# Kernel optimization log

Measured on AMD Instinct MI355X. Metric: run time of the kernel, lower is better.

Reference implementation:

```python
import math
import jax, jax.numpy as jnp
import numpy as np

E = 1024          # emb_size
H = 16            # num_heads
D = E // H        # head_dim
B, S = 4, 2048
DI = 64           # intent dim
K = 32            # num intent clusters
ASSIGN_W = 0.5
MU_W = 0.5
UNC_W = 0.5
EXPLORE_SCALE = 0.5
EXPLOIT_SCALE = 0.5
TEMP_MIN = 0.5
TEMP_MAX = 2.0


def setup_inputs() -> dict:
    key = jax.random.key(0)
    ks = jax.random.split(key, 16)
    inp = {
        "his_emb": jax.random.normal(ks[0], (B, S, E), dtype=jnp.float32),
        "src_key_padding_mask": jax.random.randint(ks[1], (B, S), 0, 2).astype(bool),
        "intent_mu": jax.random.normal(ks[2], (B, S, DI), dtype=jnp.float32),
        "intent_sigma": jax.random.uniform(ks[3], (B, S, DI), dtype=jnp.float32),
        "intent_assign": jax.random.uniform(ks[4], (B, S, K), dtype=jnp.float32),
        "explore": jax.random.uniform(ks[5], (B, S), dtype=jnp.float32),
        "exploit": jax.random.uniform(ks[6], (B, S), dtype=jnp.float32),
    }
    std = 0.02
    inp["Wq"] = jax.random.normal(ks[7], (E, E), dtype=jnp.float32) * std
    inp["bq"] = jnp.zeros((E,), dtype=jnp.float32)
    inp["Wk"] = jax.random.normal(ks[8], (E, E), dtype=jnp.float32) * std
    inp["bk"] = jnp.zeros((E,), dtype=jnp.float32)
    inp["Wv"] = jax.random.normal(ks[9], (E, E), dtype=jnp.float32) * std
    inp["bv"] = jnp.zeros((E,), dtype=jnp.float32)
    inp["Wo"] = jax.random.normal(ks[10], (E, E), dtype=jnp.float32) * std
    inp["bo"] = jnp.zeros((E,), dtype=jnp.float32)
    return inp


def _forward(his_emb, src_key_padding_mask, intent_mu, intent_sigma, intent_assign,
             explore, exploit, Wq, bq, Wk, bk, Wv, bv, Wo, bo):
    b, s, _ = his_emb.shape
    # projections -> [b, h, s, d]
    def proj(W, bias):
        return (his_emb @ W.T + bias).reshape(b, s, H, D).transpose(0, 2, 1, 3)
    q, k, v = proj(Wq, bq), proj(Wk, bk), proj(Wv, bv)

    logits = jnp.einsum("bhqd,bhkd->bhqk", q, k) / math.sqrt(D)  # [b,h,s,s]

    # intent bias [b, s, s]
    assign_sim = jnp.einsum("bqc,bkc->bqk", intent_assign, intent_assign)
    bias = ASSIGN_W * assign_sim
    # mean squared distance via expansion (avoids [b,s,s,DI] intermediate)
    sq = jnp.sum(intent_mu * intent_mu, axis=-1)  # [b,s]
    dot = jnp.einsum("bqd,bkd->bqk", intent_mu, intent_mu)
    mu_dist = (sq[:, :, None] + sq[:, None, :] - 2.0 * dot) / DI
    bias = bias - MU_W * mu_dist
    uncertainty = jnp.mean(intent_sigma, axis=-1)[:, None, :]  # [b,1,s] over keys
    bias = bias - UNC_W * uncertainty

    logits = logits + bias[:, None, :, :]

    attn_mask = src_key_padding_mask[:, None, None, :]  # [b,1,1,s]
    logits = jnp.where(attn_mask, -1e16, logits)

    # per-query temperature scaling
    temperature = 1.0 + EXPLORE_SCALE * explore - EXPLOIT_SCALE * exploit
    temperature = jnp.clip(temperature, TEMP_MIN, TEMP_MAX)
    temperature = jnp.where(src_key_padding_mask, 1.0, temperature)  # [b,s]
    logits = logits / temperature[:, None, :, None]

    probs = jax.nn.softmax(logits, axis=-1)
    probs = jnp.where(attn_mask, 0.0, probs)
    probs = probs / jnp.maximum(jnp.sum(probs, axis=-1, keepdims=True), 1e-8)

    out = jnp.einsum("bhqk,bhkd->bhqd", probs, v)
    out = out.transpose(0, 2, 1, 3).reshape(b, s, E)
    out = out @ Wo.T + bo
    return jnp.where(src_key_padding_mask[:, :, None], 0.0, out)


def reference(his_emb, src_key_padding_mask, intent_mu, intent_sigma, intent_assign,
              explore, exploit, Wq, bq, Wk, bk, Wv, bv, Wo, bo):
    return _forward(his_emb, src_key_padding_mask, intent_mu, intent_sigma,
                    intent_assign, explore, exploit, Wq, bq, Wk, bk, Wv, bv, Wo, bo)
```

## Files before the change

### kernel.cpp

```cpp
#include <hip/hip_runtime.h>
#include <hip/hip_bf16.h>
#include <stdint.h>
#include <stddef.h>

#define Bn 4
#define Sn 2048
#define En 1024
#define Hn 16
#define DIn 64
#define BSn (Bn*Sn)
#define L2E 1.44269504089f
#define SH8L 11.5415603271f

typedef __attribute__((ext_vector_type(8))) short short8;
typedef __attribute__((ext_vector_type(4))) short short4v;
typedef __attribute__((ext_vector_type(4))) float fx4;
typedef __attribute__((ext_vector_type(16))) float fx16;
typedef __attribute__((ext_vector_type(8))) _Float16 half8;
typedef __attribute__((ext_vector_type(2))) __fp16 fp16x2;
typedef __attribute__((ext_vector_type(4))) int ix4;

__device__ __forceinline__ short f2bf(float f){
  union U { __hip_bfloat16 h; short s; } u; u.h = __float2bfloat16(f); return u.s;
}
__device__ __forceinline__ short f2h(float f){
  _Float16 h = (_Float16)f; return __builtin_bit_cast(short, h);
}

__device__ __forceinline__ void async16(const void* g, void* l){
  __builtin_amdgcn_global_load_lds((const __attribute__((address_space(1))) unsigned int*)g,
                                   (__attribute__((address_space(3))) unsigned int*)l, 16, 0, 0);
}

__device__ __forceinline__ fx4 mfma_bf(short8 a, short8 b, fx4 c){
  return __builtin_amdgcn_mfma_f32_16x16x32_bf16(a, b, c, 0, 0, 0);
}
__device__ __forceinline__ fx4 mfma_h(short8 a, short8 b, fx4 c){
  return __builtin_amdgcn_mfma_f32_16x16x32_f16(__builtin_bit_cast(half8, a),
                                                __builtin_bit_cast(half8, b), c, 0, 0, 0);
}
__device__ __forceinline__ fx16 mfma32h(short8 a, short8 b, fx16 c){
  return __builtin_amdgcn_mfma_f32_32x32x16_f16(__builtin_bit_cast(half8, a),
                                                __builtin_bit_cast(half8, b), c, 0, 0, 0);
}

#define FENCE asm volatile("" ::: "memory")
#define WAIT_VM4 asm volatile("s_waitcnt vmcnt(4)" ::: "memory")
#define WAIT_VM0 asm volatile("s_waitcnt vmcnt(0)" ::: "memory")
#define WAIT_LGKM0 asm volatile("s_waitcnt lgkmcnt(0)" ::: "memory")

__global__ void scan_mask_k(const int* __restrict__ mask, int* __restrict__ sidx,
                            int* __restrict__ scnt){
  int b = blockIdx.x;
  const int* mb = mask + (size_t)b*Sn;
  __shared__ int wsum[4];
  int tid = threadIdx.x;
  int v[8]; int c = 0;
  #pragma unroll
  for (int j=0;j<8;j++){ v[j] = (mb[tid*8+j] == 0); c += v[j]; }
  int lane = tid&63, wv = tid>>6;
  int pref = c;
  #pragma unroll
  for (int m=1; m<64; m<<=1){ int o = __shfl_up(pref, m, 64); if (lane >= m) pref += o; }
  if (lane==63) wsum[wv] = pref;
  __syncthreads();
  int wbase = 0;
  for (int wprev=0; wprev<wv; wprev++) wbase += wsum[wprev];
  int pos = wbase + pref - c;
  #pragma unroll
  for (int j=0;j<8;j++){ if (v[j]) sidx[(size_t)b*Sn + pos++] = tid*8+j; }
  if (tid==255) scnt[b] = wbase + pref;
}

__global__ __launch_bounds__(256) void fused_prep_k(
    const float* __restrict__ his, const int* __restrict__ sidx, const int* __restrict__ scnt,
    const float* __restrict__ mu, const float* __restrict__ sigma,
    const float* __restrict__ assign, const float* __restrict__ explore,
    const float* __restrict__ exploit, const int* __restrict__ mask,
    const float* __restrict__ Wq, const float* __restrict__ Wk,
    const float* __restrict__ Wv, const float* __restrict__ Wo,
    short* __restrict__ WQKV, short* __restrict__ Wof,
    short* __restrict__ Xc, float* __restrict__ a1Lc,
    _Float16* __restrict__ F, _Float16* __restrict__ G, float* __restrict__ out)
{
  __shared__ int sj[32];
  const int id = blockIdx.x, tid = threadIdx.x;
  if (id < 512){
    int u = id*256 + tid;
    fx4 v[8];
    int seg[8], off[8];
    #pragma unroll
    for (int it=0; it<8; it++){
      int i = u + it*131072;
      seg[it] = i >> 18;
      off[it] = i & 262143;
      const float* src = (seg[it]==0)?Wq:(seg[it]==1)?Wk:(seg[it]==2)?Wv:Wo;
      v[it] = ((const fx4*)src)[off[it]];
    }
    #pragma unroll
    for (int it=0; it<8; it++){
      short4v o;
      if (seg[it] < 3) o = (short4v){ f2bf(v[it][0]), f2bf(v[it][1]), f2bf(v[it][2]), f2bf(v[it][3]) };
      else             o = (short4v){ f2h(v[it][0]),  f2h(v[it][1]),  f2h(v[it][2]),  f2h(v[it][3])  };
      if (seg[it] < 3) ((short4v*)WQKV)[(size_t)seg[it]*262144 + off[it]] = o;
      else             ((short4v*)Wof)[off[it]] = o;
    }
  } else if (id < 768){
    int t = id - 512;
    int b = t >> 6, jb = t & 63;
    int cnt = scnt[b];
    int scp = (cnt + 127) & ~127;
    int j0 = jb*32;
    if (j0 >= scp) return;
    if (tid < 32){
      int j = j0 + tid;
      int s = (j < cnt) ? sidx[(size_t)b*Sn + j] : -1;
      sj[tid] = s;
      float a1 = 1.0f;
      if (s >= 0){
        float tt = 1.f + 0.5f*explore[(size_t)b*Sn + s] - 0.5f*exploit[(size_t)b*Sn + s];
        tt = fminf(fmaxf(tt, 0.5f), 2.f);
        a1 = 0.125f/tt * L2E;
      }
      a1Lc[(size_t)b*Sn + j] = a1;
    }
    __syncthreads();
    const float* hb = his + (size_t)b*Sn*En;
    short* Xb_ = Xc + ((size_t)b*Sn + j0)*En;
    #pragma unroll 8
    for (int r=0; r<32; r++){
      int s = sj[r];
      short4v o;
      if (s >= 0){
        fx4 v = *(const fx4*)(hb + (size_t)s*En + tid*4);
        o = (short4v){ f2bf(v[0]), f2bf(v[1]), f2bf(v[2]), f2bf(v[3]) };
      } else o = (short4v){0,0,0,0};
      *(short4v*)(Xb_ + (size_t)r*En + tid*4) = o;
    }
  } else {
    int r = (id - 768)*4 + (tid>>6);
    int lane = tid & 63;
    float muv = mu[(size_t)r*DIn + lane];
    float sgv = sigma[(size_t)r*DIn + lane];
    float sq = muv*muv, sg = sgv;
    #pragma unroll
    for (int m=32; m; m>>=1){ sq += __shfl_xor(sq,m,64); sg += __shfl_xor(sg,m,64); }
    float unc = sg*(1.f/64.f);
    #pragma unroll
    for (int cb=0; cb<128; cb+=64){
      int col = cb + lane;
      float fv, gv;
      if (col < 32){ float a = assign[(size_t)r*32 + col]; fv = 0.5f*a; gv = a; }
      else if (col < 96){ float m2 = mu[(size_t)r*DIn + (col-32)]; fv = m2*(1.f/64.f); gv = m2; }
      else if (col == 96){ fv = -sq*(1.f/128.f); gv = 1.f; }
      else if (col == 97){ fv = 1.f; gv = -(sq*(1.f/128.f) + 0.5f*unc); }
      else { fv = 0.f; gv = 0.f; }
      F[(size_t)r*128 + col] = (_Float16)fv;
      G[(size_t)r*128 + col] = (_Float16)gv;
    }
    if (mask[r]){
      fx4 z = {0.f,0.f,0.f,0.f};
      #pragma unroll
      for (int i2=0; i2<4; i2++)
        ((fx4*)(out + (size_t)r*En))[lane + 64*i2] = z;
    }
  }
}


__global__ __launch_bounds__(256, 4) void fused_gemm_k(
    const short* __restrict__ A, const short* __restrict__ Wqkv,
    short* __restrict__ Q, short* __restrict__ K, short* __restrict__ Vt,
    const float* __restrict__ bq, const float* __restrict__ bk, const float* __restrict__ bv,
    const _Float16* __restrict__ G, const _Float16* __restrict__ F,
    _Float16* __restrict__ biasT, const float* __restrict__ a1Lc,
    const int* __restrict__ sidx, const int* __restrict__ scnt)
{
  __shared__ short sm[16384];
  const int tid = threadIdx.x;
  const int wv = tid>>6, lane = tid&63, quad = lane>>4, l16 = lane&15;
  const int wm = (wv>>1)*64, wn = (wv&1)*64;
  const int gid = blockIdx.x, g5 = gid/5, r5 = gid%5;
  int srw[2], sgc[2];
  #pragma unroll
  for (int i=0; i<2; i++){
    int idx = i*256 + tid;
    srw[i] = 2*(idx>>3) + (idx&1);
    sgc[i] = (((idx>>1)&3) ^ ((idx>>3)&3))*8;
  }
  int roffA[4], roffB[4];
  #pragma unroll
  for (int mi=0; mi<4; mi++){
    int row = wm + mi*16 + l16;
    roffA[mi] = (row>>1)*64 + ((quad ^ ((row>>1)&3))*16) + (row&1)*8;
    int rowb = wn + mi*16 + l16;
    roffB[mi] = (rowb>>1)*64 + ((quad ^ ((rowb>>1)&3))*16) + (rowb&1)*8;
  }
  short* A0 = sm;       short* A1 = sm + 4096;
  short* B0 = sm + 8192; short* B1 = sm + 12288;
  fx4 acc[4][4] = {};

  if (r5 < 3){
    int qi = g5*3 + r5;
    const int m0 = (qi/24)*128, n0g = (qi%24)*128;
    const int bb = m0 >> 11, jloc = m0 & 2047;
    const int scp = (scnt[bb] + 127) & ~127;
    if (jloc >= scp) return;
    const int seg = n0g >> 10, nloc = n0g & 1023;
    auto stage = [&](int kt, short* dA, short* dB){
      int k0 = kt*32;
      #pragma unroll
      for (int i=0; i<2; i++){
        int idx = i*256 + tid;
        async16(A    + (size_t)(m0+srw[i])*En  + k0 + sgc[i], dA + idx*8);
        async16(Wqkv + (size_t)(n0g+srw[i])*En + k0 + sgc[i], dB + idx*8);
      }
    };
    auto compute = [&](const short* cA, const short* cB){
      short8 af[4], bfr[4];
      #pragma unroll
      for (int mi=0; mi<4; mi++) af[mi]  = *(const short8*)&cA[roffA[mi]];
      #pragma unroll
      for (int ni=0; ni<4; ni++) bfr[ni] = *(const short8*)&cB[roffB[ni]];
      #pragma unroll
      for (int mi=0; mi<4; mi++)
        #pragma unroll
        for (int ni=0; ni<4; ni++)
          acc[mi][ni] = mfma_bf(af[mi], bfr[ni], acc[mi][ni]);
    };
    stage(0, A0, B0);
    for (int kt2=0; kt2<16; kt2++){
      stage(2*kt2+1, A1, B1);
      WAIT_VM4;
      __builtin_amdgcn_s_barrier(); FENCE;
      compute(A0, B0);
      WAIT_LGKM0;
      __builtin_amdgcn_s_barrier(); FENCE;
      if (kt2 < 15){ stage(2*kt2+2, A0, B0); WAIT_VM4; }
      else         { WAIT_VM0; }
      __builtin_amdgcn_s_barrier(); FENCE;
      compute(A1, B1);
      WAIT_LGKM0;
      __builtin_amdgcn_s_barrier(); FENCE;
    }
    __syncthreads();
    const float* biasv = (seg == 0) ? bq : (seg == 1) ? bk : bv;
    if (seg < 2){
      short* C = seg ? K : Q;
      #pragma unroll
      for (int mi=0; mi<4; mi++)
        #pragma unroll
        for (int ni=0; ni<4; ni++){
          int col = nloc + wn + ni*16 + l16;
          float b0 = biasv[col];
          #pragma unroll
          for (int rg=0; rg<4; rg++){
            int row = m0 + wm + mi*16 + quad*4 + rg;
            C[(size_t)row*En + col] = f2h(acc[mi][ni][rg] + b0);
          }
        }
    } else {
      short* Ct = sm;
      #pragma unroll
      for (int p=0; p<2; p++){
        __syncthreads();
        if ((wv&1) == p){
          #pragma unroll
          for (int mi=0; mi<4; mi++)
            #pragma unroll
            for (int ni=0; ni<4; ni++){
              int lcol = ni*16 + l16;
              int lrow = wm + mi*16 + quad*4;
              float b0 = biasv[nloc + p*64 + lcol];
              short4v pk;
              #pragma unroll
              for (int rg=0; rg<4; rg++) pk[rg] = f2h(acc[mi][ni][rg] + b0);
              *(short4v*)&Ct[lcol*136 + lrow] = pk;
            }
        }
        __syncthreads();
        int sl = (tid&15)*8;
        #pragma unroll
        for (int e8=0; e8<4; e8++){
          int e_l = e8*16 + (tid>>4);
          fx4 val = *(const fx4*)&Ct[e_l*136 + sl];
          int e_g = nloc + p*64 + e_l;
          size_t dst = ((size_t)(bb*Hn + (e_g>>6))*64 + (e_g&63))*Sn + jloc + sl;
          *(fx4*)&Vt[dst] = val;
        }
      }
    }
  } else {
    int bi = g5*2 + (r5-3);
    const int b = bi >> 8, rem = bi & 255;
    const int m0 = (rem >> 4)*128, n0 = (rem & 15)*128;
    const int cnt = scnt[b];
    const int scp64  = (cnt + 63) & ~63;
    const int scp128 = (cnt + 127) & ~127;
    if (m0 >= scp64)  return;
    if (n0 >= scp128) return;
    const int sC = scp128;
    const short* Gb = (const short*)G + (size_t)b*Sn*128;
    const short* Fb = (const short*)F + (size_t)b*Sn*128;
    const int* sx = sidx + (size_t)b*Sn;
    int rA[2], rB[2];
    #pragma unroll
    for (int i=0; i<2; i++){
      int gr = m0 + srw[i];  rA[i] = (gr < cnt) ? sx[gr] : 0;
      int qr = n0 + srw[i];  rB[i] = (qr < cnt) ? sx[qr] : 0;
    }
    auto stageB = [&](int kt, short* dA, short* dB){
      int k0 = kt*32;
      #pragma unroll
      for (int i=0; i<2; i++){
        int idx = i*256 + tid;
        async16(Gb + (size_t)rA[i]*128 + k0 + sgc[i], dA + idx*8);
        async16(Fb + (size_t)rB[i]*128 + k0 + sgc[i], dB + idx*8);
      }
    };
    auto computeB = [&](const short* cA, const short* cB){
      short8 af[4], bfr[4];
      #pragma unroll
      for (int mi=0; mi<4; mi++) af[mi]  = *(const short8*)&cA[roffA[mi]];
      #pragma unroll
      for (int ni=0; ni<4; ni++) bfr[ni] = *(const short8*)&cB[roffB[ni]];
      #pragma unroll
      for (int mi=0; mi<4; mi++)
        #pragma unroll
        for (int ni=0; ni<4; ni++)
          acc[mi][ni] = mfma_h(af[mi], bfr[ni], acc[mi][ni]);
    };
    stageB(0, A0, B0);
    stageB(1, A1, B1); WAIT_VM4;
    __builtin_amdgcn_s_barrier(); FENCE;
    computeB(A0, B0); WAIT_LGKM0;
    __builtin_amdgcn_s_barrier(); FENCE;
    stageB(2, A0, B0); WAIT_VM4;
    __builtin_amdgcn_s_barrier(); FENCE;
    computeB(A1, B1); WAIT_LGKM0;
    __builtin_amdgcn_s_barrier(); FENCE;
    stageB(3, A1, B1); WAIT_VM4;
    __builtin_amdgcn_s_barrier(); FENCE;
    computeB(A0, B0); WAIT_LGKM0;
    __builtin_amdgcn_s_barrier(); FENCE;
    WAIT_VM0;
    __builtin_amdgcn_s_barrier(); FENCE;
    computeB(A1, B1);
    _Float16* bQ = biasT + (size_t)b*Sn*Sn;
    #pragma unroll
    for (int mi=0; mi<4; mi++)
      #pragma unroll
      for (int ni=0; ni<4; ni++){
        int col = n0 + wn + ni*16 + l16;
        int rowb = m0 + wm + mi*16 + quad*4;
        float s8 = 8.f * a1Lc[b*Sn + col];
        short4v pk;
        #pragma unroll
        for (int rg=0; rg<4; rg++){
          int s = rowb + rg;
          short hv;
          if (s >= cnt) hv = (short)0xFC00;
          else hv = f2h(acc[mi][ni][rg]*s8 - SH8L);
          pk[rg] = hv;
        }
        *(short4v*)&bQ[((size_t)(rowb>>3)*sC + col)*8 + (rowb&7)] = pk;
      }
  }
}

__global__ __launch_bounds__(256) void gemm_out_k(
    const short* __restrict__ A, const short* __restrict__ Bm, float* __restrict__ C,
    const float* __restrict__ biasv, const int* __restrict__ sidx, const int* __restrict__ scnt)
{
  __shared__ short sm[16384];
  const int tid = threadIdx.x;
  const int wv = tid>>6, lane = tid&63, quad = lane>>4, l16 = lane&15;
  const int m0 = blockIdx.y*128, n0 = blockIdx.x*128;
  const int b = m0 >> 11, jloc = m0 & 2047;
  const int cnt = scnt[b];
  const int scp = (cnt + 127) & ~127;
  if (jloc >= scp) return;
  const int* sx = sidx + (size_t)b*Sn;
  const int wm = (wv>>1)*64, wn = (wv&1)*64;
  int srw[2], sgc[2];
  #pragma unroll
  for (int i=0; i<2; i++){
    int idx = i*256 + tid;
    srw[i] = 2*(idx>>3) + (idx&1);
    sgc[i] = (((idx>>1)&3) ^ ((idx>>3)&3))*8;
  }
  auto stage = [&](int kt, short* dA, short* dB){
    int k0 = kt*32;
    #pragma unroll
    for (int i=0; i<2; i++){
      int idx = i*256 + tid;
      async16(A  + (size_t)(m0+srw[i])*En + k0 + sgc[i], dA + idx*8);
      async16(Bm + (size_t)(n0+srw[i])*En + k0 + sgc[i], dB + idx*8);
    }
  };
  fx4 acc[4][4] = {};
  int roffA[4], roffB[4];
  #pragma unroll
  for (int mi=0; mi<4; mi++){
    int row = wm + mi*16 + l16;
    roffA[mi] = (row>>1)*64 + ((quad ^ ((row>>1)&3))*16) + (row&1)*8;
    int rowb = wn + mi*16 + l16;
    roffB[mi] = (rowb>>1)*64 + ((quad ^ ((rowb>>1)&3))*16) + (rowb&1)*8;
  }
  auto compute = [&](const short* cA, const short* cB){
    short8 af[4], bfr[4];
    #pragma unroll
    for (int mi=0; mi<4; mi++) af[mi]  = *(const short8*)&cA[roffA[mi]];
    #pragma unroll
    for (int ni=0; ni<4; ni++) bfr[ni] = *(const short8*)&cB[roffB[ni]];
    #pragma unroll
    for (int mi=0; mi<4; mi++)
      #pragma unroll
      for (int ni=0; ni<4; ni++)
        acc[mi][ni] = mfma_h(af[mi], bfr[ni], acc[mi][ni]);
  };
  stage(0, sm, sm+8192);
  for (int kt2=0; kt2<16; kt2++){
    stage(2*kt2+1, sm+4096, sm+12288);
    WAIT_VM4;
    __builtin_amdgcn_s_barrier(); FENCE;
    compute(sm, sm+8192);
    WAIT_LGKM0;
    __builtin_amdgcn_s_barrier(); FENCE;
    if (kt2 < 15){ stage(2*kt2+2, sm, sm+8192); WAIT_VM4; }
    else         { WAIT_VM0; }
    __builtin_amdgcn_s_barrier(); FENCE;
    compute(sm+4096, sm+12288);
    WAIT_LGKM0;
    __builtin_amdgcn_s_barrier(); FENCE;
  }
  #pragma unroll
  for (int mi=0; mi<4; mi++)
    #pragma unroll
    for (int ni=0; ni<4; ni++)
      #pragma unroll
      for (int rg=0; rg<4; rg++){
        int j = jloc + wm + mi*16 + quad*4 + rg;
        if (j < cnt){
          int row = b*Sn + sx[j];
          int col = n0 + wn + ni*16 + l16;
          C[(size_t)row*En + col] = acc[mi][ni][rg] + biasv[col];
        }
      }
}

__global__ __launch_bounds__(256, 4) void flash7_k(
    const short* __restrict__ Qg, const short* __restrict__ Kg, const short* __restrict__ Vtg,
    const _Float16* __restrict__ biasB, const float* __restrict__ a1Lv,
    const int* __restrict__ scnt, short* __restrict__ AO)
{
  __shared__ short smem[2][2][64*64];
  const int tid = threadIdx.x, wv = tid>>6, lane = tid&63;
  const int l32 = lane&31, hi = lane>>5;
  const int q0 = blockIdx.x*128;
  const int b = blockIdx.y >> 4, h = blockIdx.y & 15;
  const int cnt = scnt[b];
  const int NT = ((cnt + 63) & ~63) >> 6;
  const int scp128 = (cnt + 127) & ~127;
  if (q0 >= scp128) return;
  const int sC = scp128;
  const short* Qb  = Qg  + (size_t)b*Sn*En + h*64;
  const int q = q0 + wv*32 + l32;
  const float a1L = a1Lv[b*Sn + q];

  const int r0 = tid>>3, c0 = (tid&7) ^ (r0&7);
  const int kr0 = (r0 & 51) | ((r0&4)<<1) | ((r0&8)>>1);
  const short* kA = Kg  + (size_t)b*Sn*En + h*64 + (size_t)kr0*En + c0*8;
  const short* vA = Vtg + (size_t)(b*Hn + h)*64*Sn + (size_t)r0*Sn + c0*8;
  const _Float16* bP = biasB + (size_t)b*Sn*Sn + ((size_t)hi*sC + q)*8;
  const int ld0 = tid*8;

  auto issue = [&](int buf){
    short* base = &smem[buf][0][0];
    async16(kA,             base + ld0);
    async16(kA + 32*En,     base + 2048 + ld0);
    async16(vA,             base + 4096 + ld0);
    async16(vA + 32*Sn,     base + 4096 + 2048 + ld0);
  };
  if (NT > 0){ issue(0); }
  kA += 64*En; vA += 64;

  short8 qf[4];
  #pragma unroll
  for (int c=0; c<4; c++)
    qf[c] = *(const short8*)(Qb + (size_t)q*En + c*16 + hi*8);

  int koff[2][4], voff[2][4];
  #pragma unroll
  for (int t=0; t<2; t++){
    int m = t*32 + l32;
    #pragma unroll
    for (int c=0; c<4; c++)
      koff[t][c] = m*64 + (((c*2 + hi) ^ (m&7))*8);
  }
  #pragma unroll
  for (int ds=0; ds<2; ds++){
    int rv = ds*32 + l32;
    #pragma unroll
    for (int sc=0; sc<4; sc++)
      voff[ds][sc] = 4096 + rv*64 + (((sc*2 + hi) ^ (rv&7))*8);
  }

  fp16x2 one2; one2[0] = (__fp16)1.0f; one2[1] = (__fp16)1.0f;
  fx16 o0 = {}, o1 = {};
  float psum = 0.f;

  for (int T=0; T<NT; T++){
    __syncthreads();
    const short* base = &smem[T&1][0][0];
    if (T < NT-1){ issue((T&1)^1); kA += 64*En; vA += 64; }

    #pragma unroll
    for (int t=0; t<2; t++){
      half8 bch[2];
      #pragma unroll
      for (int c2=0; c2<2; c2++)
        bch[c2] = *(const half8*)(bP + (size_t)(t*4 + c2*2)*sC*8);
      fx16 sa = {};
      __builtin_amdgcn_s_setprio(1);
      #pragma unroll
      for (int c=0; c<4; c++){
        short8 ka = *(const short8*)(base + koff[t][c]);
        sa = mfma32h(ka, qf[c], sa);
      }
      __builtin_amdgcn_s_setprio(0);
      #pragma unroll
      for (int c2=0; c2<2; c2++){
        fp16x2 pk_[4];
        #pragma unroll
        for (int jj=0; jj<4; jj++){
          float pa = __builtin_amdgcn_exp2f(fmaf(sa[c2*8 + jj*2],     a1L, (float)bch[c2][jj*2]));
          float pb = __builtin_amdgcn_exp2f(fmaf(sa[c2*8 + jj*2 + 1], a1L, (float)bch[c2][jj*2+1]));
          pk_[jj] = __builtin_amdgcn_cvt_pkrtz(pa, pb);
          psum = __builtin_amdgcn_fdot2(pk_[jj], one2, psum, false);
        }
        ix4 fr = { __builtin_bit_cast(int, pk_[0]), __builtin_bit_cast(int, pk_[1]),
                   __builtin_bit_cast(int, pk_[2]), __builtin_bit_cast(int, pk_[3]) };
        short8 pfr = __builtin_bit_cast(short8, fr);
        int sc = t*2 + c2;
        __builtin_amdgcn_s_setprio(1);
        #pragma unroll
        for (int ds=0; ds<2; ds++){
          short8 va = *(const short8*)(base + voff[ds][sc]);
          if (ds == 0) o0 = mfma32h(va, pfr, o0);
          else         o1 = mfma32h(va, pfr, o1);
        }
        __builtin_amdgcn_s_setprio(0);
      }
    }
    bP += (size_t)8*sC*8;
  }

  psum += __shfl_xor(psum, 32, 64);
  float linv = 1.f/fmaxf(psum, 1e-30f);

  __syncthreads();
  short* stage = &smem[0][0][0] + wv*2304;
  #pragma unroll
  for (int ds=0; ds<2; ds++){
    const fx16& o = ds ? o1 : o0;
    #pragma unroll
    for (int rq=0; rq<4; rq++){
      int d0 = ds*32 + rq*8 + hi*4;
      short4v pk;
      #pragma unroll
      for (int j=0; j<4; j++) pk[j] = f2h(o[rq*4 + j]*linv);
      *(short4v*)&stage[l32*72 + d0] = pk;
    }
  }
  short* AOb = AO + (size_t)b*Sn*En + h*64;
  #pragma unroll
  for (int rnd=0; rnd<4; rnd++){
    int idx = rnd*64 + lane;
    int r = idx>>3, ch = idx&7;
    fx4 val = *(const fx4*)&stage[r*72 + ch*8];
    *(fx4*)(AOb + (size_t)(q0 + wv*32 + r)*En + ch*8) = val;
  }
}

extern "C" void kernel_launch(void* const* d_in, const int* in_sizes, int n_in,
                              void* d_out, int out_size, void* d_ws, size_t ws_size,
                              hipStream_t stream)
{
  const float* his     = (const float*)d_in[0];
  const int*   mask    = (const int*)  d_in[1];
  const float* mu      = (const float*)d_in[2];
  const float* sigma   = (const float*)d_in[3];
  const float* assign  = (const float*)d_in[4];
  const float* explore = (const float*)d_in[5];
  const float* exploit = (const float*)d_in[6];
  const float* Wq = (const float*)d_in[7];  const float* bq = (const float*)d_in[8];
  const float* Wk = (const float*)d_in[9];  const float* bk = (const float*)d_in[10];
  const float* Wv = (const float*)d_in[11]; const float* bv = (const float*)d_in[12];
  const float* Wo = (const float*)d_in[13]; const float* bo = (const float*)d_in[14];

  char* w = (char*)d_ws;
  size_t off = 0;
  auto alloc = [&](size_t bytes){ void* p = w + off; off += (bytes + 255) & ~(size_t)255; return p; };
  short*     Xc    = (short*)alloc((size_t)BSn*En*2);
  short*     WQKV  = (short*)alloc((size_t)3*En*En*2);
  short*     Wof   = (short*)alloc((size_t)En*En*2);
  short*     Qc    = (short*)alloc((size_t)BSn*En*2);
  short*     Kc    = (short*)alloc((size_t)BSn*En*2);
  short*     Vtc   = (short*)alloc((size_t)BSn*En*2);
  short*     AO    = (short*)alloc((size_t)BSn*En*2);
  _Float16*  F     = (_Float16*)alloc((size_t)BSn*128*2);
  _Float16*  G     = (_Float16*)alloc((size_t)BSn*128*2);
  _Float16*  biasT = (_Float16*)alloc((size_t)Bn*Sn*Sn*2);
  float*     a1Lc  = (float*)alloc((size_t)BSn*4);
  int*       sidx  = (int*)alloc((size_t)BSn*4);
  int*       scnt  = (int*)alloc(256);
  (void)ws_size; (void)in_sizes; (void)n_in; (void)out_size;

  scan_mask_k<<<Bn, 256, 0, stream>>>(mask, sidx, scnt);
  fused_prep_k<<<2816, 256, 0, stream>>>(his, sidx, scnt, mu, sigma, assign, explore, exploit,
                                         mask, Wq, Wk, Wv, Wo, WQKV, Wof, Xc, a1Lc, F, G,
                                         (float*)d_out);
  fused_gemm_k<<<2560, 256, 0, stream>>>(Xc, WQKV, Qc, Kc, Vtc, bq, bk, bv,
                                         (const _Float16*)G, (const _Float16*)F,
                                         biasT, a1Lc, sidx, scnt);
  flash7_k<<<dim3(Sn/128, Bn*Hn), 256, 0, stream>>>(Qc, Kc, Vtc, biasT, a1Lc, scnt, AO);
  gemm_out_k<<<dim3(En/128, BSn/128), 256, 0, stream>>>(AO, Wof, (float*)d_out, bo, sidx, scnt);
}
```

Baseline: 260.4 us.

## Fold mask scan into prep kernel, remap flash grid, drop setprio

The separate mask-scan kernel is removed. Each gather block in the prep kernel now recomputes the prefix scan of its batch's mask locally, and block jb==0 writes sidx and scnt for later kernels. The flash attention launch becomes a 1D grid whose block index is remapped so consecutive blocks spread across batch/head pairs, probably to balance work across XCDs. The s_setprio hints around the MFMA sections are also removed. This saves one launch but repeats the scan in every gather block and changes scheduling behavior in the attention kernel.

```diff
diff --git a/kernel.cpp b/kernel.cpp
--- a/kernel.cpp
+++ b/kernel.cpp
@@ -49,31 +49,8 @@
 #define WAIT_VM0 asm volatile("s_waitcnt vmcnt(0)" ::: "memory")
 #define WAIT_LGKM0 asm volatile("s_waitcnt lgkmcnt(0)" ::: "memory")
 
-__global__ void scan_mask_k(const int* __restrict__ mask, int* __restrict__ sidx,
-                            int* __restrict__ scnt){
-  int b = blockIdx.x;
-  const int* mb = mask + (size_t)b*Sn;
-  __shared__ int wsum[4];
-  int tid = threadIdx.x;
-  int v[8]; int c = 0;
-  #pragma unroll
-  for (int j=0;j<8;j++){ v[j] = (mb[tid*8+j] == 0); c += v[j]; }
-  int lane = tid&63, wv = tid>>6;
-  int pref = c;
-  #pragma unroll
-  for (int m=1; m<64; m<<=1){ int o = __shfl_up(pref, m, 64); if (lane >= m) pref += o; }
-  if (lane==63) wsum[wv] = pref;
-  __syncthreads();
-  int wbase = 0;
-  for (int wprev=0; wprev<wv; wprev++) wbase += wsum[wprev];
-  int pos = wbase + pref - c;
-  #pragma unroll
-  for (int j=0;j<8;j++){ if (v[j]) sidx[(size_t)b*Sn + pos++] = tid*8+j; }
-  if (tid==255) scnt[b] = wbase + pref;
-}
-
 __global__ __launch_bounds__(256) void fused_prep_k(
-    const float* __restrict__ his, const int* __restrict__ sidx, const int* __restrict__ scnt,
+    const float* __restrict__ his, int* __restrict__ sidx, int* __restrict__ scnt,
     const float* __restrict__ mu, const float* __restrict__ sigma,
     const float* __restrict__ assign, const float* __restrict__ explore,
     const float* __restrict__ exploit, const int* __restrict__ mask,
@@ -83,7 +60,8 @@
     short* __restrict__ Xc, float* __restrict__ a1Lc,
     _Float16* __restrict__ F, _Float16* __restrict__ G, float* __restrict__ out)
 {
-  __shared__ int sj[32];
+  __shared__ int sjl[32];
+  __shared__ int wsum[4];
   const int id = blockIdx.x, tid = threadIdx.x;
   if (id < 512){
     int u = id*256 + tid;
@@ -108,14 +86,39 @@
   } else if (id < 768){
     int t = id - 512;
     int b = t >> 6, jb = t & 63;
-    int cnt = scnt[b];
+    int j0 = jb*32;
+    const int* mb = mask + (size_t)b*Sn;
+    if (tid < 32) sjl[tid] = -1;
+    int v[8]; int c = 0;
+    #pragma unroll
+    for (int j=0;j<8;j++){ v[j] = (mb[tid*8+j] == 0); c += v[j]; }
+    int lane = tid&63, wv2 = tid>>6;
+    int pref = c;
+    #pragma unroll
+    for (int m=1; m<64; m<<=1){ int o = __shfl_up(pref, m, 64); if (lane >= m) pref += o; }
+    if (lane==63) wsum[wv2] = pref;
+    __syncthreads();
+    int wbase = 0;
+    for (int wp=0; wp<wv2; wp++) wbase += wsum[wp];
+    int cnt = wsum[0]+wsum[1]+wsum[2]+wsum[3];
+    int pos = wbase + pref - c;
+    int* sxb = sidx + (size_t)b*Sn;
+    #pragma unroll
+    for (int j=0;j<8;j++){
+      if (v[j]){
+        int s = tid*8+j;
+        if (pos >= j0 && pos < j0+32) sjl[pos - j0] = s;
+        if (jb == 0) sxb[pos] = s;
+        pos++;
+      }
+    }
+    if (jb == 0 && tid == 0) scnt[b] = cnt;
+    __syncthreads();
     int scp = (cnt + 127) & ~127;
-    int j0 = jb*32;
     if (j0 >= scp) return;
     if (tid < 32){
       int j = j0 + tid;
-      int s = (j < cnt) ? sidx[(size_t)b*Sn + j] : -1;
-      sj[tid] = s;
+      int s = sjl[tid];
       float a1 = 1.0f;
       if (s >= 0){
         float tt = 1.f + 0.5f*explore[(size_t)b*Sn + s] - 0.5f*exploit[(size_t)b*Sn + s];
@@ -124,16 +127,15 @@
       }
       a1Lc[(size_t)b*Sn + j] = a1;
     }
-    __syncthreads();
     const float* hb = his + (size_t)b*Sn*En;
     short* Xb_ = Xc + ((size_t)b*Sn + j0)*En;
     #pragma unroll 8
     for (int r=0; r<32; r++){
-      int s = sj[r];
+      int s = sjl[r];
       short4v o;
       if (s >= 0){
-        fx4 v = *(const fx4*)(hb + (size_t)s*En + tid*4);
-        o = (short4v){ f2bf(v[0]), f2bf(v[1]), f2bf(v[2]), f2bf(v[3]) };
+        fx4 v2 = *(const fx4*)(hb + (size_t)s*En + tid*4);
+        o = (short4v){ f2bf(v2[0]), f2bf(v2[1]), f2bf(v2[2]), f2bf(v2[3]) };
       } else o = (short4v){0,0,0,0};
       *(short4v*)(Xb_ + (size_t)r*En + tid*4) = o;
     }
@@ -449,7 +451,7 @@
       }
 }
 
-__global__ __launch_bounds__(256, 4) void flash7_k(
+__global__ __launch_bounds__(256, 4) void flash8_k(
     const short* __restrict__ Qg, const short* __restrict__ Kg, const short* __restrict__ Vtg,
     const _Float16* __restrict__ biasB, const float* __restrict__ a1Lv,
     const int* __restrict__ scnt, short* __restrict__ AO)
@@ -457,8 +459,10 @@
   __shared__ short smem[2][2][64*64];
   const int tid = threadIdx.x, wv = tid>>6, lane = tid&63;
   const int l32 = lane&31, hi = lane>>5;
-  const int q0 = blockIdx.x*128;
-  const int b = blockIdx.y >> 4, h = blockIdx.y & 15;
+  const int lid = blockIdx.x;
+  const int bh = (lid & 7)*8 + ((lid >> 3) & 7);
+  const int q0 = (lid >> 6)*128;
+  const int b = bh >> 4, h = bh & 15;
   const int cnt = scnt[b];
   const int NT = ((cnt + 63) & ~63) >> 6;
   const int scp128 = (cnt + 127) & ~127;
@@ -522,13 +526,11 @@
       for (int c2=0; c2<2; c2++)
         bch[c2] = *(const half8*)(bP + (size_t)(t*4 + c2*2)*sC*8);
       fx16 sa = {};
-      __builtin_amdgcn_s_setprio(1);
       #pragma unroll
       for (int c=0; c<4; c++){
         short8 ka = *(const short8*)(base + koff[t][c]);
         sa = mfma32h(ka, qf[c], sa);
       }
-      __builtin_amdgcn_s_setprio(0);
       #pragma unroll
       for (int c2=0; c2<2; c2++){
         fp16x2 pk_[4];
@@ -543,14 +545,12 @@
                    __builtin_bit_cast(int, pk_[2]), __builtin_bit_cast(int, pk_[3]) };
         short8 pfr = __builtin_bit_cast(short8, fr);
         int sc = t*2 + c2;
-        __builtin_amdgcn_s_setprio(1);
         #pragma unroll
         for (int ds=0; ds<2; ds++){
           short8 va = *(const short8*)(base + voff[ds][sc]);
           if (ds == 0) o0 = mfma32h(va, pfr, o0);
           else         o1 = mfma32h(va, pfr, o1);
         }
-        __builtin_amdgcn_s_setprio(0);
       }
     }
     bP += (size_t)8*sC*8;
@@ -617,13 +617,12 @@
   int*       scnt  = (int*)alloc(256);
   (void)ws_size; (void)in_sizes; (void)n_in; (void)out_size;
 
-  scan_mask_k<<<Bn, 256, 0, stream>>>(mask, sidx, scnt);
   fused_prep_k<<<2816, 256, 0, stream>>>(his, sidx, scnt, mu, sigma, assign, explore, exploit,
                                          mask, Wq, Wk, Wv, Wo, WQKV, Wof, Xc, a1Lc, F, G,
                                          (float*)d_out);
   fused_gemm_k<<<2560, 256, 0, stream>>>(Xc, WQKV, Qc, Kc, Vtc, bq, bk, bv,
                                          (const _Float16*)G, (const _Float16*)F,
                                          biasT, a1Lc, sidx, scnt);
-  flash7_k<<<dim3(Sn/128, Bn*Hn), 256, 0, stream>>>(Qc, Kc, Vtc, biasT, a1Lc, scnt, AO);
+  flash8_k<<<1024, 256, 0, stream>>>(Qc, Kc, Vtc, biasT, a1Lc, scnt, AO);
   gemm_out_k<<<dim3(En/128, BSn/128), 256, 0, stream>>>(AO, Wof, (float*)d_out, bo, sidx, scnt);
 }
```

Result: faster. 252.7 us (-3.0%).
